# Kernel tuning notes

Hardware: AMD Instinct MI355X
Metric: run time of the kernel (lower is better)

Reference implementation:

```python
import jax, jax.numpy as jnp
import numpy as np

BATCH = 8192
IN_F = 1024
OUT_F = 1024
GRID_SIZE = 5
SPLINE_ORDER = 3
GRID_LO, GRID_HI = -1.0, 1.0


def setup_inputs() -> dict:
    key = jax.random.key(0)
    k1, k2, k3, k4 = jax.random.split(key, 4)
    x = jax.random.normal(k1, (BATCH, IN_F), dtype=jnp.float32)
    # grid buffer: extended knot vector, same for every input feature
    h = (GRID_HI - GRID_LO) / GRID_SIZE
    knots = jnp.linspace(GRID_LO - SPLINE_ORDER * h, GRID_HI + SPLINE_ORDER * h,
                         GRID_SIZE + 2 * SPLINE_ORDER + 1, dtype=jnp.float32)
    grid = jnp.tile(knots[None, :], (IN_F, 1))  # [in, 12]
    fan_in_scale = 1.0 / np.sqrt(IN_F)
    base_weight = jax.random.normal(k2, (OUT_F, IN_F), dtype=jnp.float32) * fan_in_scale
    spline_weight = jax.random.normal(k3, (IN_F, GRID_SIZE + SPLINE_ORDER, OUT_F), dtype=jnp.float32) * 0.1
    spline_scaler = jax.random.normal(k4, (IN_F, OUT_F), dtype=jnp.float32) * fan_in_scale
    return {"x": x, "grid": grid, "base_weight": base_weight,
            "spline_weight": spline_weight, "spline_scaler": spline_scaler}


def b_splines(x, grid):
    """Cox-de Boor recursion. x: [B, in], grid: [in, G+2k+1] -> [B, in, G+k]."""
    xe = x[:, :, None]  # [B, in, 1]
    bases = ((xe >= grid[:, :-1]) & (xe < grid[:, 1:])).astype(x.dtype)  # [B, in, G+2k]
    for k in range(1, SPLINE_ORDER + 1):
        left = (xe - grid[:, :-(k + 1)]) / (grid[:, k:-1] - grid[:, :-(k + 1)])
        right = (grid[:, k + 1:] - xe) / (grid[:, k + 1:] - grid[:, 1:-k])
        bases = left * bases[:, :, :-1] + right * bases[:, :, 1:]
    return bases  # [B, in, G+k]


def reference(x, grid, base_weight, spline_weight, spline_scaler):
    # base branch: SiLU(x) @ W_base^T
    base_out = jax.nn.silu(x) @ base_weight.T  # [B, out]
    # spline branch
    basis = b_splines(x, grid)  # [B, in, G+k]
    scaled_w = spline_weight * spline_scaler[:, None, :]  # [in, G+k, out]
    spline_out = jnp.einsum('bik,iko->bo', basis, scaled_w)  # [B, out]
    return base_out + spline_out
```

## Files before the change

kernel.cpp:

```cpp
#include <hip/hip_runtime.h>
#include <cstdint>
#include <cstddef>

#define BATCH 8192
#define IN_F 1024
#define OUT_F 1024
#define NSPL 9
#define KDIM (IN_F * NSPL)

#define BM 256
#define BN 128
#define BK 64
#define NTILE (KDIM / BK)

typedef __bf16 bf16x8 __attribute__((ext_vector_type(8)));
typedef float f32x4 __attribute__((ext_vector_type(4)));

__device__ __forceinline__ void g2l16(const void* g, void* l) {
  __builtin_amdgcn_global_load_lds(
      (__attribute__((address_space(1))) void*)(g),
      (__attribute__((address_space(3))) void*)(l),
      16, 0, 0);
}

__device__ __forceinline__ void barrier_raw() {
  asm volatile("" ::: "memory");
  __builtin_amdgcn_s_barrier();
  asm volatile("" ::: "memory");
}

__global__ void build_w(const float* __restrict__ bw, const float* __restrict__ sw,
                        const float* __restrict__ sc, __bf16* __restrict__ Wt) {
  __shared__ float s_sw[16 * 8 * 64];
  __shared__ float s_sc[16 * 64];
  __shared__ float s_bw[64 * 16];
  const int tid = threadIdx.x;
  const int o0 = (blockIdx.x & 15) * 64;
  const int i0 = (blockIdx.x >> 4) * 16;

#pragma unroll
  for (int it = 0; it < 32; ++it) {
    const int t = it * 256 + tid;
    const int i = t >> 9, r = (t >> 6) & 7, oo = t & 63;
    s_sw[t] = sw[((size_t)(i0 + i) * 8 + r) * OUT_F + o0 + oo];
  }
#pragma unroll
  for (int it = 0; it < 4; ++it) {
    const int t = it * 256 + tid;
    const int i = t >> 6, oo = t & 63;
    s_sc[t] = sc[(size_t)(i0 + i) * OUT_F + o0 + oo];
  }
#pragma unroll
  for (int it = 0; it < 4; ++it) {
    const int t = it * 256 + tid;
    const int oo = t >> 4, ii = t & 15;
    s_bw[t] = bw[(size_t)(o0 + oo) * IN_F + i0 + ii];
  }
  __syncthreads();

  const int oo = tid >> 2;
  const int isub = (tid & 3) * 4;
#pragma unroll
  for (int is = 0; is < 4; ++is) {
    const int i = isub + is;
    __bf16* dst = Wt + (size_t)(o0 + oo) * KDIM + (size_t)(i0 + i) * NSPL;
    dst[0] = (__bf16)s_bw[oo * 16 + i];
    const float scal = s_sc[i * 64 + oo];
#pragma unroll
    for (int r = 0; r < 8; ++r)
      dst[1 + r] = (__bf16)(s_sw[i * 512 + r * 64 + oo] * scal);
  }
}

__global__ __launch_bounds__(256) void build_a(const float* __restrict__ x,
                                               __bf16* __restrict__ A) {
  __shared__ __align__(16) __bf16 rowbuf[2 * KDIM];
  const int tid = threadIdx.x;
  const int r2 = tid >> 7;
  const int tr = tid & 127;
  const size_t b = (size_t)blockIdx.x * 2 + r2;

  const float4* xp = (const float4*)(x + b * IN_F + (size_t)tr * 8);
  const float4 v0 = xp[0], v1 = xp[1];
  const float vv[8] = {v0.x, v0.y, v0.z, v0.w, v1.x, v1.y, v1.z, v1.w};

  union HB { __bf16 h[72]; uint4 q[9]; } hb;

#pragma unroll
  for (int f = 0; f < 8; ++f) {
    const float v = vv[f];
    const float s0 = v / (1.f + __expf(-v));
    const float p = (v + 2.2f) * 2.5f;
    const int cell = (int)floorf(p);
    const bool ok = (cell >= 0) && (cell <= 10) && (v < 2.2f);
    const float gate = ok ? (1.f / 6.f) : 0.f;
    const float t = p - (float)cell;
    const float t2 = t * t, t3 = t2 * t;
    const float omt = 1.f - t;
    const float c0 = gate * omt * omt * omt;
    const float c1 = gate * (3.f * t3 - 6.f * t2 + 4.f);
    const float c2 = gate * (-3.f * t3 + 3.f * t2 + 3.f * t + 1.f);
    const float c3 = gate * t3;
    const int j0 = cell - 3;
    hb.h[f * 9 + 0] = (__bf16)s0;
#pragma unroll
    for (int r = 0; r < 8; ++r) {
      const int d = r - j0;
      float val = (d == 0) ? c0 : 0.f;
      val = (d == 1) ? c1 : val;
      val = (d == 2) ? c2 : val;
      val = (d == 3) ? c3 : val;
      hb.h[f * 9 + 1 + r] = (__bf16)val;
    }
  }

  uint4* ldst = (uint4*)(rowbuf + (size_t)r2 * KDIM) + (size_t)tr * 9;
#pragma unroll
  for (int k = 0; k < 9; ++k) ldst[k] = hb.q[k];
  __syncthreads();

  const uint4* src = (const uint4*)rowbuf;
  uint4* dst = (uint4*)(A + (size_t)blockIdx.x * 2 * KDIM);
#pragma unroll
  for (int it = 0; it < 9; ++it)
    dst[it * 256 + tid] = src[it * 256 + tid];
}

__global__ __launch_bounds__(512, 2) void gemm_bt(const __bf16* __restrict__ A,
                                                  const __bf16* __restrict__ W,
                                                  float* __restrict__ out) {
  __shared__ __align__(16) __bf16 As[3][BM * BK];
  __shared__ __align__(16) __bf16 Bs[3][BN * BK];

  const int tid = threadIdx.x;
  const int wv = tid >> 6;
  const int lane = tid & 63;

  const int bid = blockIdx.x;
  const int xcd = bid & 7;
  const int j = bid >> 3;
  const int m0 = (xcd * 4 + (j & 3)) * BM;
  const int n0 = (j >> 2) * BN;

  const int wr = wv >> 1;
  const int wc = wv & 1;

  const int srow = lane >> 3;
  const int usrc = (lane & 7) ^ srow;
  const __bf16* gA = A + (size_t)(m0 + wv * 32 + srow) * KDIM + usrc * 8;
  const __bf16* gB = W + (size_t)(n0 + wv * 16 + srow) * KDIM + usrc * 8;

#define STAGE3_FIRST(q, tt)                                          \
  do {                                                               \
    const size_t ko = (size_t)(tt) * BK;                             \
    g2l16(gA + ko,                      &As[q][(wv * 32 + 0) * BK]); \
    g2l16(gA + ko + 8 * (size_t)KDIM,   &As[q][(wv * 32 + 8) * BK]); \
    g2l16(gB + ko,                      &Bs[q][(wv * 16 + 0) * BK]); \
  } while (0)
#define STAGE3_SECOND(q, tt)                                          \
  do {                                                                \
    const size_t ko = (size_t)(tt) * BK;                              \
    g2l16(gA + ko + 16 * (size_t)KDIM, &As[q][(wv * 32 + 16) * BK]);  \
    g2l16(gA + ko + 24 * (size_t)KDIM, &As[q][(wv * 32 + 24) * BK]);  \
    g2l16(gB + ko + 8 * (size_t)KDIM,  &Bs[q][(wv * 16 + 8) * BK]);   \
  } while (0)

  const int mrow = lane & 15;
  const int quad = lane >> 4;
  int aoff[4], boff[4];
#pragma unroll
  for (int mt = 0; mt < 4; ++mt) aoff[mt] = (wr * 64 + mt * 16 + mrow) * BK;
#pragma unroll
  for (int nt = 0; nt < 4; ++nt) boff[nt] = (wc * 64 + nt * 16 + mrow) * BK;
  const int colx0 = ((quad) ^ (mrow & 7)) * 8;
  const int colx1 = ((4 + quad) ^ (mrow & 7)) * 8;

  f32x4 acc[4][4];
  const f32x4 zero = {0.f, 0.f, 0.f, 0.f};
#pragma unroll
  for (int mt = 0; mt < 4; ++mt)
#pragma unroll
    for (int nt = 0; nt < 4; ++nt) acc[mt][nt] = zero;

  STAGE3_FIRST(0, 0);
  STAGE3_SECOND(0, 0);
  STAGE3_FIRST(1, 1);
  STAGE3_SECOND(1, 1);
  asm volatile("s_waitcnt vmcnt(6)" ::: "memory");
  barrier_raw();

  int q = 0;
  for (int t = 0; t < NTILE; ++t) {
    const int qp = (q == 0) ? 2 : q - 1;

    bf16x8 a0[4], b0[4];
#pragma unroll
    for (int mt = 0; mt < 4; ++mt) a0[mt] = *(const bf16x8*)(&As[q][aoff[mt] + colx0]);
#pragma unroll
    for (int nt = 0; nt < 4; ++nt) b0[nt] = *(const bf16x8*)(&Bs[q][boff[nt] + colx0]);
    if (t + 2 < NTILE) STAGE3_FIRST(qp, t + 2);
    barrier_raw();
    __builtin_amdgcn_s_setprio(1);
#pragma unroll
    for (int mt = 0; mt < 4; ++mt)
#pragma unroll
      for (int nt = 0; nt < 4; ++nt)
        acc[mt][nt] = __builtin_amdgcn_mfma_f32_16x16x32_bf16(a0[mt], b0[nt],
                                                              acc[mt][nt], 0, 0, 0);
    __builtin_amdgcn_s_setprio(0);
    barrier_raw();

    bf16x8 a1[4], b1[4];
#pragma unroll
    for (int mt = 0; mt < 4; ++mt) a1[mt] = *(const bf16x8*)(&As[q][aoff[mt] + colx1]);
#pragma unroll
    for (int nt = 0; nt < 4; ++nt) b1[nt] = *(const bf16x8*)(&Bs[q][boff[nt] + colx1]);
    if (t + 2 < NTILE) {
      STAGE3_SECOND(qp, t + 2);
      asm volatile("s_waitcnt vmcnt(6)" ::: "memory");
    } else {
      asm volatile("s_waitcnt vmcnt(0)" ::: "memory");
    }
    barrier_raw();
    __builtin_amdgcn_s_setprio(1);
#pragma unroll
    for (int mt = 0; mt < 4; ++mt)
#pragma unroll
      for (int nt = 0; nt < 4; ++nt)
        acc[mt][nt] = __builtin_amdgcn_mfma_f32_16x16x32_bf16(a1[mt], b1[nt],
                                                              acc[mt][nt], 0, 0, 0);
    __builtin_amdgcn_s_setprio(0);
    barrier_raw();

    q = (q == 2) ? 0 : q + 1;
  }

#pragma unroll
  for (int mt = 0; mt < 4; ++mt) {
#pragma unroll
    for (int nt = 0; nt < 4; ++nt) {
      const int col = n0 + wc * 64 + nt * 16 + mrow;
      const int rbase = m0 + wr * 64 + mt * 16 + quad * 4;
#pragma unroll
      for (int r = 0; r < 4; ++r)
        out[(size_t)(rbase + r) * OUT_F + col] = acc[mt][nt][r];
    }
  }
#undef STAGE3_FIRST
#undef STAGE3_SECOND
}

extern "C" void kernel_launch(void* const* d_in, const int* in_sizes, int n_in,
                              void* d_out, int out_size, void* d_ws, size_t ws_size,
                              hipStream_t stream) {
  const float* x  = (const float*)d_in[0];
  const float* bw = (const float*)d_in[2];
  const float* sw = (const float*)d_in[3];
  const float* sc = (const float*)d_in[4];
  float* out = (float*)d_out;

  __bf16* Wt = (__bf16*)d_ws;
  __bf16* Ab = (__bf16*)((char*)d_ws +
                         (size_t)OUT_F * KDIM * sizeof(__bf16));

  build_w<<<1024, 256, 0, stream>>>(bw, sw, sc, Wt);
  build_a<<<BATCH / 2, 256, 0, stream>>>(x, Ab);
  gemm_bt<<<(BATCH / BM) * (OUT_F / BN), 512, 0, stream>>>(Ab, Wt, out);
}
```

Measured before the change: 289.5 us.

## Use 256x256 GEMM tiles with split-K of two and a reduction kernel

The GEMM tile grows from 256x128 to 256x256, so each wave holds an 8x4 grid of MFMA accumulators. The K dimension is split in two, and the block count stays at 256. The staging becomes a 4-deep pipeline of 32-wide K slices with a new swizzle. The second K half writes to a workspace buffer, and an extra reduce_add kernel adds it into the output. The aim is higher arithmetic intensity per loaded byte, at the cost of a large accumulator register footprint under launch_bounds(512,2), an extra 32MB partial write plus read, and an extra launch.

```diff
diff --git a/kernel.cpp b/kernel.cpp
--- a/kernel.cpp
+++ b/kernel.cpp
@@ -9,9 +9,9 @@
 #define KDIM (IN_F * NSPL)
 
 #define BM 256
-#define BN 128
-#define BK 64
-#define NTILE (KDIM / BK)
+#define BN 256
+#define KS (KDIM / 2)
+#define NH (KS / 32)
 
 typedef __bf16 bf16x8 __attribute__((ext_vector_type(8)));
 typedef float f32x4 __attribute__((ext_vector_type(4)));
@@ -128,9 +128,10 @@
 
 __global__ __launch_bounds__(512, 2) void gemm_bt(const __bf16* __restrict__ A,
                                                   const __bf16* __restrict__ W,
-                                                  float* __restrict__ out) {
-  __shared__ __align__(16) __bf16 As[3][BM * BK];
-  __shared__ __align__(16) __bf16 Bs[3][BN * BK];
+                                                  float* __restrict__ out,
+                                                  float* __restrict__ part) {
+  __shared__ __align__(16) __bf16 As[4][BM * 32];
+  __shared__ __align__(16) __bf16 Bs[4][BN * 32];
 
   const int tid = threadIdx.x;
   const int wv = tid >> 6;
@@ -140,114 +141,106 @@
   const int xcd = bid & 7;
   const int j = bid >> 3;
   const int m0 = (xcd * 4 + (j & 3)) * BM;
-  const int n0 = (j >> 2) * BN;
-
-  const int wr = wv >> 1;
-  const int wc = wv & 1;
-
-  const int srow = lane >> 3;
-  const int usrc = (lane & 7) ^ srow;
-  const __bf16* gA = A + (size_t)(m0 + wv * 32 + srow) * KDIM + usrc * 8;
-  const __bf16* gB = W + (size_t)(n0 + wv * 16 + srow) * KDIM + usrc * 8;
-
-#define STAGE3_FIRST(q, tt)                                          \
-  do {                                                               \
-    const size_t ko = (size_t)(tt) * BK;                             \
-    g2l16(gA + ko,                      &As[q][(wv * 32 + 0) * BK]); \
-    g2l16(gA + ko + 8 * (size_t)KDIM,   &As[q][(wv * 32 + 8) * BK]); \
-    g2l16(gB + ko,                      &Bs[q][(wv * 16 + 0) * BK]); \
-  } while (0)
-#define STAGE3_SECOND(q, tt)                                          \
+  const int n0 = ((j >> 2) & 3) * BN;
+  const int ks = j >> 4;
+  const size_t kbase = (size_t)ks * KS;
+
+  const int wr = wv >> 2;
+  const int wc = wv & 3;
+
+  const int srow = lane >> 2;
+  const int usrc = (lane & 3) ^ ((lane >> 3) & 3);
+  const __bf16* gA = A + (size_t)(m0 + wv * 32 + srow) * KDIM + kbase + usrc * 8;
+  const __bf16* gB = W + (size_t)(n0 + wv * 32 + srow) * KDIM + kbase + usrc * 8;
+
+#define STAGE_HALF(s, hh)                                             \
   do {                                                                \
-    const size_t ko = (size_t)(tt) * BK;                              \
-    g2l16(gA + ko + 16 * (size_t)KDIM, &As[q][(wv * 32 + 16) * BK]);  \
-    g2l16(gA + ko + 24 * (size_t)KDIM, &As[q][(wv * 32 + 24) * BK]);  \
-    g2l16(gB + ko + 8 * (size_t)KDIM,  &Bs[q][(wv * 16 + 8) * BK]);   \
+    const size_t ko = (size_t)(hh) * 32;                              \
+    g2l16(gA + ko,                     &As[s][wv * 1024]);            \
+    g2l16(gA + ko + 16 * (size_t)KDIM, &As[s][wv * 1024 + 512]);      \
+    g2l16(gB + ko,                     &Bs[s][wv * 1024]);            \
+    g2l16(gB + ko + 16 * (size_t)KDIM, &Bs[s][wv * 1024 + 512]);      \
   } while (0)
 
   const int mrow = lane & 15;
   const int quad = lane >> 4;
-  int aoff[4], boff[4];
-#pragma unroll
-  for (int mt = 0; mt < 4; ++mt) aoff[mt] = (wr * 64 + mt * 16 + mrow) * BK;
-#pragma unroll
-  for (int nt = 0; nt < 4; ++nt) boff[nt] = (wc * 64 + nt * 16 + mrow) * BK;
-  const int colx0 = ((quad) ^ (mrow & 7)) * 8;
-  const int colx1 = ((4 + quad) ^ (mrow & 7)) * 8;
-
-  f32x4 acc[4][4];
+  const int xu = (quad ^ ((mrow >> 1) & 3)) * 8;
+  int aoff[8], boff[4];
+#pragma unroll
+  for (int mt = 0; mt < 8; ++mt) aoff[mt] = (wr * 128 + mt * 16 + mrow) * 32 + xu;
+#pragma unroll
+  for (int nt = 0; nt < 4; ++nt) boff[nt] = (wc * 64 + nt * 16 + mrow) * 32 + xu;
+
+  f32x4 acc[8][4];
   const f32x4 zero = {0.f, 0.f, 0.f, 0.f};
 #pragma unroll
-  for (int mt = 0; mt < 4; ++mt)
+  for (int mt = 0; mt < 8; ++mt)
 #pragma unroll
     for (int nt = 0; nt < 4; ++nt) acc[mt][nt] = zero;
 
-  STAGE3_FIRST(0, 0);
-  STAGE3_SECOND(0, 0);
-  STAGE3_FIRST(1, 1);
-  STAGE3_SECOND(1, 1);
-  asm volatile("s_waitcnt vmcnt(6)" ::: "memory");
+  STAGE_HALF(0, 0);
+  STAGE_HALF(1, 1);
+  STAGE_HALF(2, 2);
+  asm volatile("s_waitcnt vmcnt(8)" ::: "memory");
   barrier_raw();
 
-  int q = 0;
-  for (int t = 0; t < NTILE; ++t) {
-    const int qp = (q == 0) ? 2 : q - 1;
-
-    bf16x8 a0[4], b0[4];
-#pragma unroll
-    for (int mt = 0; mt < 4; ++mt) a0[mt] = *(const bf16x8*)(&As[q][aoff[mt] + colx0]);
-#pragma unroll
-    for (int nt = 0; nt < 4; ++nt) b0[nt] = *(const bf16x8*)(&Bs[q][boff[nt] + colx0]);
-    if (t + 2 < NTILE) STAGE3_FIRST(qp, t + 2);
-    barrier_raw();
-    __builtin_amdgcn_s_setprio(1);
-#pragma unroll
-    for (int mt = 0; mt < 4; ++mt)
-#pragma unroll
-      for (int nt = 0; nt < 4; ++nt)
-        acc[mt][nt] = __builtin_amdgcn_mfma_f32_16x16x32_bf16(a0[mt], b0[nt],
-                                                              acc[mt][nt], 0, 0, 0);
-    __builtin_amdgcn_s_setprio(0);
-    barrier_raw();
-
-    bf16x8 a1[4], b1[4];
-#pragma unroll
-    for (int mt = 0; mt < 4; ++mt) a1[mt] = *(const bf16x8*)(&As[q][aoff[mt] + colx1]);
-#pragma unroll
-    for (int nt = 0; nt < 4; ++nt) b1[nt] = *(const bf16x8*)(&Bs[q][boff[nt] + colx1]);
-    if (t + 2 < NTILE) {
-      STAGE3_SECOND(qp, t + 2);
-      asm volatile("s_waitcnt vmcnt(6)" ::: "memory");
+  for (int h = 0; h < NH; ++h) {
+    const int s = h & 3;
+
+    bf16x8 af[8], bf[4];
+#pragma unroll
+    for (int mt = 0; mt < 8; ++mt) af[mt] = *(const bf16x8*)(&As[s][aoff[mt]]);
+#pragma unroll
+    for (int nt = 0; nt < 4; ++nt) bf[nt] = *(const bf16x8*)(&Bs[s][boff[nt]]);
+
+    if (h + 3 < NH) {
+      STAGE_HALF((h + 3) & 3, h + 3);
+      asm volatile("s_waitcnt vmcnt(8)" ::: "memory");
+    } else if (h + 2 < NH) {
+      asm volatile("s_waitcnt vmcnt(4)" ::: "memory");
     } else {
       asm volatile("s_waitcnt vmcnt(0)" ::: "memory");
     }
     barrier_raw();
+
     __builtin_amdgcn_s_setprio(1);
 #pragma unroll
-    for (int mt = 0; mt < 4; ++mt)
+    for (int mt = 0; mt < 8; ++mt)
 #pragma unroll
       for (int nt = 0; nt < 4; ++nt)
-        acc[mt][nt] = __builtin_amdgcn_mfma_f32_16x16x32_bf16(a1[mt], b1[nt],
+        acc[mt][nt] = __builtin_amdgcn_mfma_f32_16x16x32_bf16(af[mt], bf[nt],
                                                               acc[mt][nt], 0, 0, 0);
     __builtin_amdgcn_s_setprio(0);
     barrier_raw();
-
-    q = (q == 2) ? 0 : q + 1;
-  }
-
-#pragma unroll
-  for (int mt = 0; mt < 4; ++mt) {
+  }
+
+  float* __restrict__ dst = ks ? part : out;
+#pragma unroll
+  for (int mt = 0; mt < 8; ++mt) {
 #pragma unroll
     for (int nt = 0; nt < 4; ++nt) {
       const int col = n0 + wc * 64 + nt * 16 + mrow;
-      const int rbase = m0 + wr * 64 + mt * 16 + quad * 4;
+      const int rbase = m0 + wr * 128 + mt * 16 + quad * 4;
 #pragma unroll
       for (int r = 0; r < 4; ++r)
-        out[(size_t)(rbase + r) * OUT_F + col] = acc[mt][nt][r];
+        dst[(size_t)(rbase + r) * OUT_F + col] = acc[mt][nt][r];
     }
   }
-#undef STAGE3_FIRST
-#undef STAGE3_SECOND
+#undef STAGE_HALF
+}
+
+__global__ __launch_bounds__(256) void reduce_add(float* __restrict__ out,
+                                                  const float* __restrict__ part) {
+  const size_t base = (size_t)blockIdx.x * 256 + threadIdx.x;
+  f32x4* o = (f32x4*)out;
+  const f32x4* p = (const f32x4*)part;
+#pragma unroll
+  for (int it = 0; it < 4; ++it) {
+    const size_t i = base + (size_t)it * 2048 * 256;
+    f32x4 a = o[i], b = p[i];
+    a.x += b.x; a.y += b.y; a.z += b.z; a.w += b.w;
+    o[i] = a;
+  }
 }
 
 extern "C" void kernel_launch(void* const* d_in, const int* in_sizes, int n_in,
@@ -262,8 +255,12 @@
   __bf16* Wt = (__bf16*)d_ws;
   __bf16* Ab = (__bf16*)((char*)d_ws +
                          (size_t)OUT_F * KDIM * sizeof(__bf16));
+  float* part = (float*)((char*)d_ws +
+                         (size_t)OUT_F * KDIM * sizeof(__bf16) +
+                         (size_t)BATCH * KDIM * sizeof(__bf16));
 
   build_w<<<1024, 256, 0, stream>>>(bw, sw, sc, Wt);
   build_a<<<BATCH / 2, 256, 0, stream>>>(x, Ab);
-  gemm_bt<<<(BATCH / BM) * (OUT_F / BN), 512, 0, stream>>>(Ab, Wt, out);
-}
+  gemm_bt<<<(BATCH / BM) * (OUT_F / BN) * 2, 512, 0, stream>>>(Ab, Wt, out, part);
+  reduce_add<<<2048, 256, 0, stream>>>(out, part);
+}
```

Measured after the change: 291.2 us. About the same (+0.6%).
